# Kernel optimization log

Hardware: AMD Instinct MI355X
Metric: run time of the kernel (lower is better)

The kernel has to match this reference:

```python
import jax, jax.numpy as jnp
import numpy as np

DATA_STD = np.array([0.229, 0.224, 0.225], dtype=np.float32)
DATA_SCALING = float(1.0 / DATA_STD.min())  # 1.0 / np.min(data_std)

B, C, D = 4096, 1000, 2048


def setup_inputs() -> dict:
    key = jax.random.key(0)
    k1, k2, k3 = jax.random.split(key, 3)
    prediction = jax.random.normal(k1, (B, C), dtype=jnp.float32)
    W = jax.random.normal(k2, (C, D), dtype=jnp.float32) * 0.02
    K = jax.random.uniform(k3, (1,), dtype=jnp.float32) + 0.5  # lipschitz estimate scalar
    return {"prediction": prediction, "W": W, "K": K}


def reference(prediction, W, K):
    # K = model.lipschitz_estimate / Kfc * data_scaling
    k = K[0] * DATA_SCALING
    kW = k * W                                   # [C, D]
    y_j, j = jax.lax.top_k(prediction, 2)        # values [B,2], indices [B,2]
    j0 = j[:, 0]                                 # [B] top-1 class index
    kW_j = kW[j0]                                # [B, D] gathered rows
    # Kij[b, c] = || kW_j[b] - kW[c] ||_2, computed via the GEMM expansion
    # (avoids materializing the [B, D, C] difference tensor)
    sq_j = jnp.sum(kW_j * kW_j, axis=1, keepdims=True)   # [B, 1]
    sq_w = jnp.sum(kW * kW, axis=1)[None, :]             # [1, C]
    cross = kW_j @ kW.T                                  # [B, C]
    Kij = jnp.sqrt(jnp.maximum(sq_j + sq_w - 2.0 * cross, 0.0))
    margins = y_j[:, :1] - prediction                    # [B, C]
    onehot = j0[:, None] == jnp.arange(prediction.shape[1])[None, :]
    # torch scatters inf into margins at the top-1 column; there Kij==0 and
    # inf/0 == inf, so setting ratios directly to inf is the same forward math.
    safe_Kij = jnp.where(onehot, 1.0, Kij)
    ratios = jnp.where(onehot, jnp.inf, margins / safe_Kij)
    return jnp.min(ratios, axis=1)                       # [B]
```

## Files before the change

### kernel.cpp

```cpp
#include <hip/hip_runtime.h>
#include <hip/hip_bf16.h>

#define B_ROWS 4096
#define C_CLS  1000
#define D_DIM  2048
#define NPAD   1024

typedef __attribute__((ext_vector_type(8))) short s16x8;
typedef __attribute__((ext_vector_type(4))) float f32x4;

__device__ __forceinline__ unsigned short f2bf(float f) {
    __hip_bfloat16 h = __float2bfloat16(f);
    unsigned short u;
    __builtin_memcpy(&u, &h, 2);
    return u;
}

__global__ __launch_bounds__(256) void prep_kernel(const float* __restrict__ W,
                                                   unsigned short* __restrict__ Wb,
                                                   float* __restrict__ sqw) {
    const int row = blockIdx.x;
    const int tid = threadIdx.x;
    unsigned short* wrow = Wb + (size_t)row * D_DIM;
    if (row >= C_CLS) {
        uint4 z; z.x = z.y = z.z = z.w = 0u;
        *reinterpret_cast<uint4*>(wrow + tid * 8) = z;
        if (tid == 0) sqw[row] = 0.f;
        return;
    }
    const float* wr = W + (size_t)row * D_DIM;
    float4 x0 = *reinterpret_cast<const float4*>(wr + tid * 8);
    float4 x1 = *reinterpret_cast<const float4*>(wr + tid * 8 + 4);
    float s = x0.x * x0.x + x0.y * x0.y + x0.z * x0.z + x0.w * x0.w
            + x1.x * x1.x + x1.y * x1.y + x1.z * x1.z + x1.w * x1.w;
    union { unsigned short u[8]; uint4 v; } pk;
    pk.u[0] = f2bf(x0.x); pk.u[1] = f2bf(x0.y); pk.u[2] = f2bf(x0.z); pk.u[3] = f2bf(x0.w);
    pk.u[4] = f2bf(x1.x); pk.u[5] = f2bf(x1.y); pk.u[6] = f2bf(x1.z); pk.u[7] = f2bf(x1.w);
    *reinterpret_cast<uint4*>(wrow + tid * 8) = pk.v;
#pragma unroll
    for (int off = 32; off > 0; off >>= 1) s += __shfl_down(s, off);
    __shared__ float sv[4];
    const int lane = tid & 63, wid = tid >> 6;
    if (lane == 0) sv[wid] = s;
    __syncthreads();
    if (tid == 0) sqw[row] = sv[0] + sv[1] + sv[2] + sv[3];
}

__global__ __launch_bounds__(512) void dist_kernel(const unsigned short* __restrict__ Wb,
                                                   const float* __restrict__ sqw,
                                                   const float* __restrict__ Kin,
                                                   float* __restrict__ dist) {
    __shared__ unsigned short smem[4][2][64 * 64];

    const int tid  = threadIdx.x;
    const int lane = tid & 63;
    const int wid  = tid >> 6;
    const int wm   = wid >> 1;
    const int wn   = wid & 1;
    const int l16  = lane & 15;
    const int quad = lane >> 4;

    const int b  = blockIdx.x;
    const int rg = b & 7, s = b >> 3;
    const int by = (rg >> 1) * 4 + (s >> 3);
    const int bx = (rg & 1) * 8 + (s & 7);

    const int srow = wid * 8 + (lane >> 3);
    const int scol = (((lane & 7) ^ (lane >> 3)) << 3);
    const unsigned short* gA = Wb + (size_t)(by * 64 + srow) * D_DIM + scol;
    const unsigned short* gB = Wb + (size_t)(bx * 64 + srow) * D_DIM + scol;

#define STAGE(bufi, kk)                                                                 \
    do {                                                                                \
        __builtin_amdgcn_global_load_lds(                                               \
            (const __attribute__((address_space(1))) void*)(gA + (kk)),                 \
            (__attribute__((address_space(3))) void*)&smem[bufi][0][wid * 512], 16, 0, 0); \
        __builtin_amdgcn_global_load_lds(                                               \
            (const __attribute__((address_space(1))) void*)(gB + (kk)),                 \
            (__attribute__((address_space(3))) void*)&smem[bufi][1][wid * 512], 16, 0, 0); \
    } while (0)

    f32x4 acc0 = {0.f, 0.f, 0.f, 0.f};
    f32x4 acc1 = {0.f, 0.f, 0.f, 0.f};

    STAGE(0, 0);
    STAGE(1, 64);
    STAGE(2, 128);

    const int arow  = (wm * 16 + l16) * 64;
    const int brow0 = (wn * 32 + l16) * 64;
    const int brow1 = (wn * 32 + 16 + l16) * 64;

    for (int t = 0; t < 32; ++t) {
        if (t < 30)       asm volatile("s_waitcnt vmcnt(4)" ::: "memory");
        else if (t == 30) asm volatile("s_waitcnt vmcnt(2)" ::: "memory");
        else              asm volatile("s_waitcnt vmcnt(0)" ::: "memory");
        __builtin_amdgcn_s_barrier();
        asm volatile("" ::: "memory");

        if (t < 29) STAGE((t + 3) & 3, (t + 3) * 64);

        const unsigned short* Ab = &smem[t & 3][0][0];
        const unsigned short* Bb = &smem[t & 3][1][0];
        s16x8 a[2], b0[2], b1[2];
#pragma unroll
        for (int ks = 0; ks < 2; ++ks) {
            const int cs = ((((ks << 2) | quad) ^ (lane & 7)) << 3);
            a[ks]  = *reinterpret_cast<const s16x8*>(Ab + arow  + cs);
            b0[ks] = *reinterpret_cast<const s16x8*>(Bb + brow0 + cs);
            b1[ks] = *reinterpret_cast<const s16x8*>(Bb + brow1 + cs);
        }
#pragma unroll
        for (int ks = 0; ks < 2; ++ks) {
            acc0 = __builtin_amdgcn_mfma_f32_16x16x32_bf16(a[ks], b0[ks], acc0, 0, 0, 0);
            acc1 = __builtin_amdgcn_mfma_f32_16x16x32_bf16(a[ks], b1[ks], acc1, 0, 0, 0);
        }
    }
#undef STAGE

    const float kscale = Kin[0] * 4.4642857142857144f;

    f32x4 accs[2] = {acc0, acc1};
#pragma unroll
    for (int nt = 0; nt < 2; ++nt) {
#pragma unroll
        for (int r = 0; r < 4; ++r) {
            const int ga = by * 64 + wm * 16 + quad * 4 + r;
            const int gc = bx * 64 + wn * 32 + nt * 16 + l16;
            float d2 = sqw[ga] + sqw[gc] - 2.0f * accs[nt][r];
            dist[(size_t)ga * NPAD + gc] = kscale * sqrtf(fmaxf(d2, 0.f));
        }
    }
}

__global__ __launch_bounds__(256) void final_kernel(const float* __restrict__ pred,
                                                    const float* __restrict__ dist,
                                                    float* __restrict__ out) {
    const int row = blockIdx.x;
    const int tid = threadIdx.x;
    const int lane = tid & 63, wid = tid >> 6;
    __shared__ float sp[C_CLS];
    __shared__ float sv[4];
    __shared__ int   si[4];

    const float* p = pred + (size_t)row * C_CLS;
    float v = -INFINITY;
    int bi = 0x7fffffff;
    if (tid < 250) {
        float4 x = *reinterpret_cast<const float4*>(p + tid * 4);
        const int c0 = tid * 4;
        sp[c0 + 0] = x.x; sp[c0 + 1] = x.y; sp[c0 + 2] = x.z; sp[c0 + 3] = x.w;
        v = x.x; bi = c0;
        if (x.y > v) { v = x.y; bi = c0 + 1; }
        if (x.z > v) { v = x.z; bi = c0 + 2; }
        if (x.w > v) { v = x.w; bi = c0 + 3; }
    }
#pragma unroll
    for (int off = 32; off > 0; off >>= 1) {
        float ov = __shfl_down(v, off);
        int   oi = __shfl_down(bi, off);
        if (ov > v || (ov == v && oi < bi)) { v = ov; bi = oi; }
    }
    if (lane == 0) { sv[wid] = v; si[wid] = bi; }
    __syncthreads();
    float y0 = sv[0]; int j0 = si[0];
#pragma unroll
    for (int w = 1; w < 4; ++w) {
        if (sv[w] > y0 || (sv[w] == y0 && si[w] < j0)) { y0 = sv[w]; j0 = si[w]; }
    }

    const float* drow = dist + (size_t)j0 * NPAD;
    float rmin = INFINITY;
    if (tid < 250) {
        const int c0 = tid * 4;
        float4 dv = *reinterpret_cast<const float4*>(drow + c0);
        float4 pv = *reinterpret_cast<const float4*>(&sp[c0]);
        if (c0 + 0 != j0) rmin = fminf(rmin, (y0 - pv.x) * __builtin_amdgcn_rcpf(dv.x));
        if (c0 + 1 != j0) rmin = fminf(rmin, (y0 - pv.y) * __builtin_amdgcn_rcpf(dv.y));
        if (c0 + 2 != j0) rmin = fminf(rmin, (y0 - pv.z) * __builtin_amdgcn_rcpf(dv.z));
        if (c0 + 3 != j0) rmin = fminf(rmin, (y0 - pv.w) * __builtin_amdgcn_rcpf(dv.w));
    }
#pragma unroll
    for (int off = 32; off > 0; off >>= 1) rmin = fminf(rmin, __shfl_down(rmin, off));
    __syncthreads();
    if (lane == 0) sv[wid] = rmin;
    __syncthreads();
    if (tid == 0) out[row] = fminf(fminf(sv[0], sv[1]), fminf(sv[2], sv[3]));
}

extern "C" void kernel_launch(void* const* d_in, const int* in_sizes, int n_in,
                              void* d_out, int out_size, void* d_ws, size_t ws_size,
                              hipStream_t stream) {
    const float* pred = (const float*)d_in[0];
    const float* W    = (const float*)d_in[1];
    const float* K    = (const float*)d_in[2];
    float* out = (float*)d_out;

    char* ws = (char*)d_ws;
    unsigned short* Wb = (unsigned short*)ws;
    float* dist = (float*)(ws + (size_t)NPAD * D_DIM * 2);
    float* sqw  = (float*)(ws + (size_t)NPAD * D_DIM * 2 + (size_t)NPAD * NPAD * 4);

    prep_kernel<<<NPAD, 256, 0, stream>>>(W, Wb, sqw);
    dist_kernel<<<dim3(256), 512, 0, stream>>>(Wb, sqw, K, dist);
    final_kernel<<<B_ROWS, 256, 0, stream>>>(pred, dist, out);
}
```

Measured before the change: 87.02 us.

## Split K across wave groups with 32x32 per-wave tiles and LDS reduction

Reorganizes the dist GEMM block so the eight waves form two K-slice groups, each wave computing a 32x32 sub-tile over half of every 64-wide K step. Each wave now reads two A and two B fragments for four MFMAs instead of three fragments per two MFMAs, raising the LDS-read-to-MFMA reuse ratio. Partial sums from the second K group are reduced through shared memory at the end, which adds a barrier and LDS traffic in the epilogue, and only half the waves run the epilogue.

```diff
diff --git a/kernel.cpp b/kernel.cpp
--- a/kernel.cpp
+++ b/kernel.cpp
@@ -55,8 +55,10 @@
     const int tid  = threadIdx.x;
     const int lane = tid & 63;
     const int wid  = tid >> 6;
-    const int wm   = wid >> 1;
-    const int wn   = wid & 1;
+    const int ksl  = wid >> 2;
+    const int wsub = wid & 3;
+    const int wm   = wsub >> 1;
+    const int wn   = wsub & 1;
     const int l16  = lane & 15;
     const int quad = lane >> 4;
 
@@ -80,16 +82,20 @@
             (__attribute__((address_space(3))) void*)&smem[bufi][1][wid * 512], 16, 0, 0); \
     } while (0)
 
-    f32x4 acc0 = {0.f, 0.f, 0.f, 0.f};
-    f32x4 acc1 = {0.f, 0.f, 0.f, 0.f};
+    f32x4 acc00 = {0.f, 0.f, 0.f, 0.f};
+    f32x4 acc01 = {0.f, 0.f, 0.f, 0.f};
+    f32x4 acc10 = {0.f, 0.f, 0.f, 0.f};
+    f32x4 acc11 = {0.f, 0.f, 0.f, 0.f};
 
     STAGE(0, 0);
     STAGE(1, 64);
     STAGE(2, 128);
 
-    const int arow  = (wm * 16 + l16) * 64;
+    const int arow0 = (wm * 32 + l16) * 64;
+    const int arow1 = (wm * 32 + 16 + l16) * 64;
     const int brow0 = (wn * 32 + l16) * 64;
     const int brow1 = (wn * 32 + 16 + l16) * 64;
+    const int cs = (((ksl * 4 + quad) ^ (lane & 7)) << 3);
 
     for (int t = 0; t < 32; ++t) {
         if (t < 30)       asm volatile("s_waitcnt vmcnt(4)" ::: "memory");
@@ -102,33 +108,48 @@
 
         const unsigned short* Ab = &smem[t & 3][0][0];
         const unsigned short* Bb = &smem[t & 3][1][0];
-        s16x8 a[2], b0[2], b1[2];
-#pragma unroll
-        for (int ks = 0; ks < 2; ++ks) {
-            const int cs = ((((ks << 2) | quad) ^ (lane & 7)) << 3);
-            a[ks]  = *reinterpret_cast<const s16x8*>(Ab + arow  + cs);
-            b0[ks] = *reinterpret_cast<const s16x8*>(Bb + brow0 + cs);
-            b1[ks] = *reinterpret_cast<const s16x8*>(Bb + brow1 + cs);
-        }
-#pragma unroll
-        for (int ks = 0; ks < 2; ++ks) {
-            acc0 = __builtin_amdgcn_mfma_f32_16x16x32_bf16(a[ks], b0[ks], acc0, 0, 0, 0);
-            acc1 = __builtin_amdgcn_mfma_f32_16x16x32_bf16(a[ks], b1[ks], acc1, 0, 0, 0);
-        }
+        s16x8 a0 = *reinterpret_cast<const s16x8*>(Ab + arow0 + cs);
+        s16x8 a1 = *reinterpret_cast<const s16x8*>(Ab + arow1 + cs);
+        s16x8 b0 = *reinterpret_cast<const s16x8*>(Bb + brow0 + cs);
+        s16x8 b1 = *reinterpret_cast<const s16x8*>(Bb + brow1 + cs);
+        acc00 = __builtin_amdgcn_mfma_f32_16x16x32_bf16(a0, b0, acc00, 0, 0, 0);
+        acc01 = __builtin_amdgcn_mfma_f32_16x16x32_bf16(a0, b1, acc01, 0, 0, 0);
+        acc10 = __builtin_amdgcn_mfma_f32_16x16x32_bf16(a1, b0, acc10, 0, 0, 0);
+        acc11 = __builtin_amdgcn_mfma_f32_16x16x32_bf16(a1, b1, acc11, 0, 0, 0);
     }
 #undef STAGE
 
-    const float kscale = Kin[0] * 4.4642857142857144f;
-
-    f32x4 accs[2] = {acc0, acc1};
-#pragma unroll
-    for (int nt = 0; nt < 2; ++nt) {
-#pragma unroll
-        for (int r = 0; r < 4; ++r) {
-            const int ga = by * 64 + wm * 16 + quad * 4 + r;
-            const int gc = bx * 64 + wn * 32 + nt * 16 + l16;
-            float d2 = sqw[ga] + sqw[gc] - 2.0f * accs[nt][r];
-            dist[(size_t)ga * NPAD + gc] = kscale * sqrtf(fmaxf(d2, 0.f));
+    __syncthreads();
+    float* fs = reinterpret_cast<float*>(&smem[0][0][0]);
+    if (wid >= 4) {
+        float* dst = fs + (size_t)(wid - 4) * 1024 + lane * 16;
+        *reinterpret_cast<f32x4*>(dst + 0)  = acc00;
+        *reinterpret_cast<f32x4*>(dst + 4)  = acc01;
+        *reinterpret_cast<f32x4*>(dst + 8)  = acc10;
+        *reinterpret_cast<f32x4*>(dst + 12) = acc11;
+    }
+    __syncthreads();
+    if (wid < 4) {
+        const float* src = fs + (size_t)wid * 1024 + lane * 16;
+        acc00 += *reinterpret_cast<const f32x4*>(src + 0);
+        acc01 += *reinterpret_cast<const f32x4*>(src + 4);
+        acc10 += *reinterpret_cast<const f32x4*>(src + 8);
+        acc11 += *reinterpret_cast<const f32x4*>(src + 12);
+
+        const float kscale = Kin[0] * 4.4642857142857144f;
+        f32x4 accs[2][2] = {{acc00, acc01}, {acc10, acc11}};
+#pragma unroll
+        for (int mt = 0; mt < 2; ++mt) {
+#pragma unroll
+            for (int nt = 0; nt < 2; ++nt) {
+#pragma unroll
+                for (int r = 0; r < 4; ++r) {
+                    const int ga = by * 64 + wm * 32 + mt * 16 + quad * 4 + r;
+                    const int gc = bx * 64 + wn * 32 + nt * 16 + l16;
+                    float d2 = sqw[ga] + sqw[gc] - 2.0f * accs[mt][nt][r];
+                    dist[(size_t)ga * NPAD + gc] = kscale * sqrtf(fmaxf(d2, 0.f));
+                }
+            }
         }
     }
 }
```

Result: no change. 88.08 us (+1.2%).

## Split-K the Gram GEMM across two blocks and finish distance in final kernel

Applied to the files above, without the earlier changes.

The 1024x1024 Gram GEMM is split along K into two halves, doubling the grid from 256 to 512 blocks to fill more CUs. Each half writes raw partial dot products to its own buffer, and the sqrt/norm/scale epilogue moves into the final kernel, which sums the two partials for the selected row only. This trades extra buffer writes and a second row read per output row for better GPU occupancy in the GEMM stage.

```diff
diff --git a/kernel.cpp b/kernel.cpp
--- a/kernel.cpp
+++ b/kernel.cpp
@@ -47,9 +47,7 @@
 }
 
 __global__ __launch_bounds__(512) void dist_kernel(const unsigned short* __restrict__ Wb,
-                                                   const float* __restrict__ sqw,
-                                                   const float* __restrict__ Kin,
-                                                   float* __restrict__ dist) {
+                                                   float* __restrict__ dbuf) {
     __shared__ unsigned short smem[4][2][64 * 64];
 
     const int tid  = threadIdx.x;
@@ -60,15 +58,18 @@
     const int l16  = lane & 15;
     const int quad = lane >> 4;
 
-    const int b  = blockIdx.x;
-    const int rg = b & 7, s = b >> 3;
-    const int by = (rg >> 1) * 4 + (s >> 3);
-    const int bx = (rg & 1) * 8 + (s & 7);
+    const int b    = blockIdx.x;
+    const int rg   = b & 7, s = b >> 3;
+    const int kset = s & 1;
+    const int tidx = s >> 1;
+    const int by   = (rg >> 1) * 4 + (tidx >> 3);
+    const int bx   = (rg & 1) * 8 + (tidx & 7);
+    const int kbase = kset * 1024;
 
     const int srow = wid * 8 + (lane >> 3);
     const int scol = (((lane & 7) ^ (lane >> 3)) << 3);
-    const unsigned short* gA = Wb + (size_t)(by * 64 + srow) * D_DIM + scol;
-    const unsigned short* gB = Wb + (size_t)(bx * 64 + srow) * D_DIM + scol;
+    const unsigned short* gA = Wb + (size_t)(by * 64 + srow) * D_DIM + kbase + scol;
+    const unsigned short* gB = Wb + (size_t)(bx * 64 + srow) * D_DIM + kbase + scol;
 
 #define STAGE(bufi, kk)                                                                 \
     do {                                                                                \
@@ -91,14 +92,14 @@
     const int brow0 = (wn * 32 + l16) * 64;
     const int brow1 = (wn * 32 + 16 + l16) * 64;
 
-    for (int t = 0; t < 32; ++t) {
-        if (t < 30)       asm volatile("s_waitcnt vmcnt(4)" ::: "memory");
-        else if (t == 30) asm volatile("s_waitcnt vmcnt(2)" ::: "memory");
+    for (int t = 0; t < 16; ++t) {
+        if (t < 14)       asm volatile("s_waitcnt vmcnt(4)" ::: "memory");
+        else if (t == 14) asm volatile("s_waitcnt vmcnt(2)" ::: "memory");
         else              asm volatile("s_waitcnt vmcnt(0)" ::: "memory");
         __builtin_amdgcn_s_barrier();
         asm volatile("" ::: "memory");
 
-        if (t < 29) STAGE((t + 3) & 3, (t + 3) * 64);
+        if (t < 13) STAGE((t + 3) & 3, (t + 3) * 64);
 
         const unsigned short* Ab = &smem[t & 3][0][0];
         const unsigned short* Bb = &smem[t & 3][1][0];
@@ -118,8 +119,7 @@
     }
 #undef STAGE
 
-    const float kscale = Kin[0] * 4.4642857142857144f;
-
+    float* dst = dbuf + (size_t)kset * NPAD * NPAD;
     f32x4 accs[2] = {acc0, acc1};
 #pragma unroll
     for (int nt = 0; nt < 2; ++nt) {
@@ -127,14 +127,15 @@
         for (int r = 0; r < 4; ++r) {
             const int ga = by * 64 + wm * 16 + quad * 4 + r;
             const int gc = bx * 64 + wn * 32 + nt * 16 + l16;
-            float d2 = sqw[ga] + sqw[gc] - 2.0f * accs[nt][r];
-            dist[(size_t)ga * NPAD + gc] = kscale * sqrtf(fmaxf(d2, 0.f));
+            dst[(size_t)ga * NPAD + gc] = accs[nt][r];
         }
     }
 }
 
 __global__ __launch_bounds__(256) void final_kernel(const float* __restrict__ pred,
-                                                    const float* __restrict__ dist,
+                                                    const float* __restrict__ dbuf,
+                                                    const float* __restrict__ sqw,
+                                                    const float* __restrict__ Kin,
                                                     float* __restrict__ out) {
     const int row = blockIdx.x;
     const int tid = threadIdx.x;
@@ -169,16 +170,35 @@
         if (sv[w] > y0 || (sv[w] == y0 && si[w] < j0)) { y0 = sv[w]; j0 = si[w]; }
     }
 
-    const float* drow = dist + (size_t)j0 * NPAD;
+    const float kscale = Kin[0] * 4.4642857142857144f;
+    const float inv_ks = 1.0f / kscale;
+    const float sqj = sqw[j0];
+    const float* d0 = dbuf + (size_t)j0 * NPAD;
+    const float* d1 = dbuf + (size_t)NPAD * NPAD + (size_t)j0 * NPAD;
+
     float rmin = INFINITY;
     if (tid < 250) {
         const int c0 = tid * 4;
-        float4 dv = *reinterpret_cast<const float4*>(drow + c0);
+        float4 a  = *reinterpret_cast<const float4*>(d0 + c0);
+        float4 b  = *reinterpret_cast<const float4*>(d1 + c0);
+        float4 sq = *reinterpret_cast<const float4*>(sqw + c0);
         float4 pv = *reinterpret_cast<const float4*>(&sp[c0]);
-        if (c0 + 0 != j0) rmin = fminf(rmin, (y0 - pv.x) * __builtin_amdgcn_rcpf(dv.x));
-        if (c0 + 1 != j0) rmin = fminf(rmin, (y0 - pv.y) * __builtin_amdgcn_rcpf(dv.y));
-        if (c0 + 2 != j0) rmin = fminf(rmin, (y0 - pv.z) * __builtin_amdgcn_rcpf(dv.z));
-        if (c0 + 3 != j0) rmin = fminf(rmin, (y0 - pv.w) * __builtin_amdgcn_rcpf(dv.w));
+        if (c0 + 0 != j0) {
+            float d2 = sqj + sq.x - 2.0f * (a.x + b.x);
+            rmin = fminf(rmin, (y0 - pv.x) * inv_ks * __builtin_amdgcn_rsqf(fmaxf(d2, 0.f)));
+        }
+        if (c0 + 1 != j0) {
+            float d2 = sqj + sq.y - 2.0f * (a.y + b.y);
+            rmin = fminf(rmin, (y0 - pv.y) * inv_ks * __builtin_amdgcn_rsqf(fmaxf(d2, 0.f)));
+        }
+        if (c0 + 2 != j0) {
+            float d2 = sqj + sq.z - 2.0f * (a.z + b.z);
+            rmin = fminf(rmin, (y0 - pv.z) * inv_ks * __builtin_amdgcn_rsqf(fmaxf(d2, 0.f)));
+        }
+        if (c0 + 3 != j0) {
+            float d2 = sqj + sq.w - 2.0f * (a.w + b.w);
+            rmin = fminf(rmin, (y0 - pv.w) * inv_ks * __builtin_amdgcn_rsqf(fmaxf(d2, 0.f)));
+        }
     }
 #pragma unroll
     for (int off = 32; off > 0; off >>= 1) rmin = fminf(rmin, __shfl_down(rmin, off));
@@ -198,10 +218,10 @@
 
     char* ws = (char*)d_ws;
     unsigned short* Wb = (unsigned short*)ws;
-    float* dist = (float*)(ws + (size_t)NPAD * D_DIM * 2);
-    float* sqw  = (float*)(ws + (size_t)NPAD * D_DIM * 2 + (size_t)NPAD * NPAD * 4);
+    float* dbuf = (float*)(ws + (size_t)NPAD * D_DIM * 2);
+    float* sqw  = (float*)(ws + (size_t)NPAD * D_DIM * 2 + 2 * (size_t)NPAD * NPAD * 4);
 
     prep_kernel<<<NPAD, 256, 0, stream>>>(W, Wb, sqw);
-    dist_kernel<<<dim3(256), 512, 0, stream>>>(Wb, sqw, K, dist);
-    final_kernel<<<B_ROWS, 256, 0, stream>>>(pred, dist, out);
-}
+    dist_kernel<<<dim3(512), 512, 0, stream>>>(Wb, dbuf);
+    final_kernel<<<B_ROWS, 256, 0, stream>>>(pred, dbuf, sqw, K, out);
+}
```

Measured after the change: 85.82 us. About the same (-1.4%).
